# Optimization experiments

Measured on AMD Instinct MI355X. Metric: run time of the kernel, lower is better.

The kernel has to match this reference:

```python
import jax, jax.numpy as jnp
import numpy as np

EMBED_DIM = 1024
NUM_HEADS = 16
HEAD_DIM = EMBED_DIM // NUM_HEADS
SCALE = HEAD_DIM ** 0.5


def setup_inputs() -> dict:
    key = jax.random.key(0)
    kx, kq, kk, kv, ko = jax.random.split(key, 5)
    B, S, D = 4, 2048, EMBED_DIM
    std = 1.0 / np.sqrt(D)
    return {
        "x": jax.random.normal(kx, (B, S, D), dtype=jnp.float32),
        "W_q": jax.random.normal(kq, (D, D), dtype=jnp.float32) * std,
        "W_k": jax.random.normal(kk, (D, D), dtype=jnp.float32) * std,
        "W_v": jax.random.normal(kv, (D, D), dtype=jnp.float32) * std,
        "W_o": jax.random.normal(ko, (D, D), dtype=jnp.float32) * std,
    }


def reference(x, W_q, W_k, W_v, W_o):
    B, S, D = x.shape
    H, Hd = NUM_HEADS, HEAD_DIM

    def split(t):  # [B,S,D] -> [B,H,S,Hd]
        return t.reshape(B, S, H, Hd).transpose(0, 2, 1, 3)

    # nn.Linear stores weight as [out,in] and computes x @ W.T
    Q = split(x @ W_q.T)
    K = split(x @ W_k.T)
    V = split(x @ W_v.T)

    scores = jnp.einsum("bhqd,bhkd->bhqk", Q, K) / SCALE
    causal = jnp.tril(jnp.ones((S, S), dtype=bool))
    scores = jnp.where(causal, scores, -jnp.inf)
    weights = jax.nn.softmax(scores, axis=-1)  # dropout p=0 (eval)
    out = jnp.einsum("bhqk,bhkd->bhqd", weights, V)
    out = out.transpose(0, 2, 1, 3).reshape(B, S, D)
    return out @ W_o.T
```

## Files before the change

kernel.cpp:

```cpp
#include <hip/hip_runtime.h>
#include <stdint.h>

#define DEV __device__ __forceinline__

typedef __bf16 bf16x8 __attribute__((ext_vector_type(8)));
typedef float f32x4 __attribute__((ext_vector_type(4)));

DEV ushort f2bf(float f) {
    union { float f; uint32_t u; } v; v.f = f;
    uint32_t r = v.u + 0x7FFFu + ((v.u >> 16) & 1u);
    return (ushort)(r >> 16);
}

DEV ushort bfc(float f) {
    union { __bf16 h; ushort u; } v;
    v.h = (__bf16)f;
    return v.u;
}

DEV void gld16(const void* g, void* lds) {
    __builtin_amdgcn_global_load_lds(
        (const __attribute__((address_space(1))) void*)g,
        (__attribute__((address_space(3))) void*)lds, 16, 0, 0);
}

DEV bf16x8 ld_frag(const void* p) { return *(const bf16x8*)p; }

__global__ void cvt_kernel(const float* __restrict__ in, ushort* __restrict__ out, int n4) {
    int i = blockIdx.x * blockDim.x + threadIdx.x;
    if (i >= n4) return;
    float4 v = ((const float4*)in)[i];
    ushort4 o;
    o.x = f2bf(v.x); o.y = f2bf(v.y); o.z = f2bf(v.z); o.w = f2bf(v.w);
    ((ushort4*)out)[i] = o;
}

__global__ void cvt4_kernel(const float* __restrict__ w0, const float* __restrict__ w1,
                            const float* __restrict__ w2, const float* __restrict__ w3,
                            ushort* __restrict__ out, int n4) {
    int i = blockIdx.x * blockDim.x + threadIdx.x;
    if (i >= n4) return;
    const float* src = (blockIdx.y == 0) ? w0 : (blockIdx.y == 1) ? w1
                     : (blockIdx.y == 2) ? w2 : w3;
    float4 v = ((const float4*)src)[i];
    ushort4 o;
    o.x = f2bf(v.x); o.y = f2bf(v.y); o.z = f2bf(v.z); o.w = f2bf(v.w);
    ((ushort4*)(out + (size_t)blockIdx.y * n4 * 4))[i] = o;
}

template<int F32OUT>
__global__ __launch_bounds__(256) void gemm_bt(const ushort* __restrict__ A,
                                               const ushort* __restrict__ B,
                                               void* __restrict__ C,
                                               int M, int N, int K) {
    __shared__ __align__(16) ushort As[128 * 64];
    __shared__ __align__(16) ushort Bs[128 * 64];
    const int G = gridDim.x;
    const int bid = blockIdx.x;
    const int swz = (bid & 7) * (G >> 3) + (bid >> 3);
    const int bm = swz & 63, bn = swz >> 6;
    const int t = threadIdx.x, l = t & 63, w = t >> 6;
    const int wm = w >> 1, wn = w & 1;
    const int rA = l & 15, cc = l >> 4;
    f32x4 acc[4][4] = {};

    for (int k0 = 0; k0 < K; k0 += 64) {
#pragma unroll
        for (int i = 0; i < 4; ++i) {
            int o = (w * 4 + i) * 1024 + l * 16;
            int row = o >> 7, ch = (o >> 4) & 7;
            int cs = ch ^ (row & 7);
            const char* ga = (const char*)A + (((size_t)(bm * 128 + row)) * K + k0) * 2 + cs * 16;
            gld16(ga, (char*)As + (w * 4 + i) * 1024);
            const char* gb = (const char*)B + (((size_t)(bn * 128 + row)) * K + k0) * 2 + cs * 16;
            gld16(gb, (char*)Bs + (w * 4 + i) * 1024);
        }
        __syncthreads();
        bf16x8 af[4][2], bfr[4][2];
#pragma unroll
        for (int i = 0; i < 4; ++i) {
#pragma unroll
            for (int kc = 0; kc < 2; ++kc) {
                int ra = wm * 64 + i * 16 + rA;
                int ca = (kc * 4 + cc) ^ (ra & 7);
                af[i][kc] = ld_frag((const char*)As + ra * 128 + ca * 16);
                int rb = wn * 64 + i * 16 + rA;
                int cb = (kc * 4 + cc) ^ (rb & 7);
                bfr[i][kc] = ld_frag((const char*)Bs + rb * 128 + cb * 16);
            }
        }
#pragma unroll
        for (int kc = 0; kc < 2; ++kc)
#pragma unroll
            for (int i = 0; i < 4; ++i)
#pragma unroll
                for (int j = 0; j < 4; ++j)
                    acc[i][j] = __builtin_amdgcn_mfma_f32_16x16x32_bf16(
                        af[i][kc], bfr[j][kc], acc[i][j], 0, 0, 0);
        __syncthreads();
    }
#pragma unroll
    for (int i = 0; i < 4; ++i)
#pragma unroll
        for (int j = 0; j < 4; ++j)
#pragma unroll
            for (int r = 0; r < 4; ++r) {
                int row = bm * 128 + wm * 64 + i * 16 + cc * 4 + r;
                int col = bn * 128 + wn * 64 + j * 16 + rA;
                if (F32OUT) ((float*)C)[(size_t)row * N + col] = acc[i][j][r];
                else        ((ushort*)C)[(size_t)row * N + col] = f2bf(acc[i][j][r]);
            }
}

__global__ __launch_bounds__(256) void vtrans_kernel(const ushort* __restrict__ qkv,
                                                     ushort* __restrict__ vt) {
    __shared__ ushort tile[64][68];
    const int st = blockIdx.x, bh = blockIdx.y;
    const int b = bh >> 4, h = bh & 15;
    const int t = threadIdx.x;
    const ushort* src = qkv + (size_t)(b * 2048 + st * 64) * 3072 + 2048 + h * 64;
#pragma unroll
    for (int i = 0; i < 2; ++i) {
        int idx = t + i * 256;
        int s = idx >> 3, d0 = (idx & 7) * 8;
        uint4 v = *(const uint4*)(src + (size_t)s * 3072 + d0);
        *(uint2*)&tile[s][d0]     = make_uint2(v.x, v.y);
        *(uint2*)&tile[s][d0 + 4] = make_uint2(v.z, v.w);
    }
    __syncthreads();
    ushort* dst = vt + (size_t)bh * 64 * 2048 + st * 64;
#pragma unroll
    for (int i = 0; i < 2; ++i) {
        int idx = t + i * 256;
        int d = idx >> 3, s0 = (idx & 7) * 8;
        ushort tmp[8];
#pragma unroll
        for (int j = 0; j < 8; ++j) tmp[j] = tile[s0 + j][d];
        *(uint4*)(dst + (size_t)d * 2048 + s0) = *(uint4*)tmp;
    }
}

DEV void stage_kv(const char* Kg0, const char* Vg0, int kv0,
                  char* KsB, char* VsB, int t) {
    int row = t >> 3;
    int cs = (t & 7) ^ (row & 7);
    gld16(Kg0 + (size_t)(kv0 + row) * 6144 + cs * 16, KsB + t * 16);
    gld16(Vg0 + (size_t)row * 4096 + (size_t)kv0 * 2 + cs * 16, VsB + t * 16);
}

DEV void attn_tile(const char* KsB, const char* VsB, char* PsW,
                   const bf16x8* qf, f32x4* oacc, float& lsum,
                   int rA, int cc, int qg, int kv0, bool diag) {
    f32x4 s[4] = {};
    __builtin_amdgcn_s_setprio(1);
#pragma unroll
    for (int kc = 0; kc < 2; ++kc)
#pragma unroll
        for (int c = 0; c < 4; ++c) {
            int rk = c * 16 + rA;
            int ck = (kc * 4 + cc) ^ (rk & 7);
            bf16x8 ak = ld_frag(KsB + rk * 128 + ck * 16);
            s[c] = __builtin_amdgcn_mfma_f32_16x16x32_bf16(ak, qf[kc], s[c], 0, 0, 0);
        }
    __builtin_amdgcn_s_setprio(0);
    const float SC = 0.18033688011116013f;
    const int swz = (rA & 7) << 4;
#pragma unroll
    for (int c = 0; c < 4; ++c) {
        float pv[4];
#pragma unroll
        for (int r = 0; r < 4; ++r) {
            float v = s[c][r] * SC;
            if (diag && (kv0 + c * 16 + cc * 4 + r > qg)) v = -1e30f;
            pv[r] = __builtin_amdgcn_exp2f(v);
            lsum += pv[r];
        }
        union { ushort us[4]; uint2 u2; } pk;
        pk.us[0] = bfc(pv[0]); pk.us[1] = bfc(pv[1]);
        pk.us[2] = bfc(pv[2]); pk.us[3] = bfc(pv[3]);
        *(uint2*)(PsW + rA * 128 + ((32 * c + 8 * cc) ^ swz)) = pk.u2;
    }
    bf16x8 ap[2];
    ap[0] = ld_frag(PsW + rA * 128 + ((16 * cc) ^ swz));
    ap[1] = ld_frag(PsW + rA * 128 + ((64 + 16 * cc) ^ swz));
    __builtin_amdgcn_s_setprio(1);
#pragma unroll
    for (int kc = 0; kc < 2; ++kc)
#pragma unroll
        for (int g = 0; g < 4; ++g) {
            int rv = g * 16 + rA;
            int cv = (kc * 4 + cc) ^ (rv & 7);
            bf16x8 av = ld_frag(VsB + rv * 128 + cv * 16);
            oacc[g] = __builtin_amdgcn_mfma_f32_16x16x32_bf16(av, ap[kc], oacc[g], 0, 0, 0);
        }
    __builtin_amdgcn_s_setprio(0);
}

__global__ __launch_bounds__(512, 4) void attn_kernel(const ushort* __restrict__ qkv,
                                                      const ushort* __restrict__ vt,
                                                      ushort* __restrict__ o_out) {
    const int i = blockIdx.x;
    const int xcd = i & 7, slot = i >> 3;
    const int p = slot >> 3;
    const int bh = ((slot & 7) << 3) | xcd;
    const int ftq = 15 - p;
    const int b = bh >> 4, h = bh & 15;
    const int t = threadIdx.x, l = t & 63, w = t >> 6;
    const int rA = l & 15, cc = l >> 4;
    const int wq16 = w * 16;

    __shared__ __align__(16) ushort Ks[2][64 * 64];
    __shared__ __align__(16) ushort Vs[2][64 * 64];
    __shared__ __align__(16) ushort Ps[8][16 * 64];

    const size_t xbase = (size_t)(b * 2048) * 3072 + (size_t)h * 64;
    const char* Kg0 = (const char*)(qkv + xbase + 1024);
    const char* Vg0 = (const char*)(vt + (size_t)bh * 64 * 2048);

    const int qgN = p * 128 + wq16 + rA;
    const int qgF = ftq * 128 + wq16 + rA;

    bf16x8 qfN[2], qfF[2];
    {
        const ushort* qpN = qkv + xbase + (size_t)qgN * 3072;
        const ushort* qpF = qkv + xbase + (size_t)qgF * 3072;
        qfN[0] = *(const bf16x8*)(qpN + cc * 8);
        qfN[1] = *(const bf16x8*)(qpN + 32 + cc * 8);
        qfF[0] = *(const bf16x8*)(qpF + cc * 8);
        qfF[1] = *(const bf16x8*)(qpF + 32 + cc * 8);
    }
    f32x4 oN[4] = {}, oF[4] = {};
    float lN = 0.f, lF = 0.f;

    const int nkv = 32 - 2 * p;
    stage_kv(Kg0, Vg0, 0, (char*)Ks[0], (char*)Vs[0], t);
    asm volatile("s_waitcnt vmcnt(0)" ::: "memory");
    __builtin_amdgcn_s_barrier();

    for (int kt = 0; kt < nkv; ++kt) {
        const int cur = kt & 1;
        if (kt + 1 < nkv)
            stage_kv(Kg0, Vg0, (kt + 1) * 64, (char*)Ks[cur ^ 1], (char*)Vs[cur ^ 1], t);
        const char* KsB = (const char*)Ks[cur];
        const char* VsB = (const char*)Vs[cur];
        attn_tile(KsB, VsB, (char*)Ps[w], qfF, oF, lF, rA, cc, qgF, kt * 64, kt >= nkv - 2);
        if (kt <= 2 * p + 1)
            attn_tile(KsB, VsB, (char*)Ps[w], qfN, oN, lN, rA, cc, qgN, kt * 64, kt >= 2 * p);
        asm volatile("s_waitcnt vmcnt(0)" ::: "memory");
        __builtin_amdgcn_s_barrier();
    }

    float lf = lF; lf += __shfl_xor(lf, 16); lf += __shfl_xor(lf, 32);
    float ln = lN; ln += __shfl_xor(ln, 16); ln += __shfl_xor(ln, 32);
    const float rf = 1.0f / lf, rn = 1.0f / ln;
    const size_t obF = (size_t)(b * 2048 + qgF) * 1024 + h * 64;
    const size_t obN = (size_t)(b * 2048 + qgN) * 1024 + h * 64;
#pragma unroll
    for (int g = 0; g < 4; ++g) {
        union { ushort us[4]; uint2 u2; } pf, pn;
#pragma unroll
        for (int r = 0; r < 4; ++r) {
            pf.us[r] = bfc(oF[g][r] * rf);
            pn.us[r] = bfc(oN[g][r] * rn);
        }
        *(uint2*)(o_out + obF + 16 * g + 4 * cc) = pf.u2;
        *(uint2*)(o_out + obN + 16 * g + 4 * cc) = pn.u2;
    }
}

extern "C" void kernel_launch(void* const* d_in, const int* in_sizes, int n_in,
                              void* d_out, int out_size, void* d_ws, size_t ws_size,
                              hipStream_t stream) {
    const float* x  = (const float*)d_in[0];
    const float* Wq = (const float*)d_in[1];
    const float* Wk = (const float*)d_in[2];
    const float* Wv = (const float*)d_in[3];
    const float* Wo = (const float*)d_in[4];
    float* out = (float*)d_out;

    const int M = 8192, D = 1024;
    char* ws = (char*)d_ws;
    ushort* xo_bf = (ushort*)ws;
    ushort* wqkv  = (ushort*)(ws + (size_t)M * D * 2);
    ushort* wo_bf = (ushort*)(ws + (size_t)M * D * 2 + (size_t)3 * D * D * 2);
    ushort* qkv   = (ushort*)(ws + (size_t)M * D * 2 + (size_t)4 * D * D * 2);
    ushort* vt    = (ushort*)d_out;

    cvt_kernel<<<dim3(M * D / 4 / 256), 256, 0, stream>>>(x, xo_bf, M * D / 4);
    cvt4_kernel<<<dim3(D * D / 4 / 256, 4), 256, 0, stream>>>(Wq, Wk, Wv, Wo, wqkv, D * D / 4);

    gemm_bt<0><<<dim3((M / 128) * (3072 / 128)), 256, 0, stream>>>(xo_bf, wqkv, qkv, M, 3072, D);

    vtrans_kernel<<<dim3(32, 64), 256, 0, stream>>>(qkv, vt);

    attn_kernel<<<dim3(512), 512, 0, stream>>>(qkv, vt, xo_bf);

    gemm_bt<1><<<dim3((M / 128) * (D / 128)), 256, 0, stream>>>(xo_bf, wo_bf, out, M, D, D);
}
```

Measured before the change: 258.3 us.

## Use 256x256-tile double-buffered GEMM for QKV projection

Adds a new gemm256 kernel with 512 threads, 256x256 output tiles, and double-buffered LDS. Each K-tile's global loads are interleaved in four quarters between the MFMA phases, with swizzled LDS addresses. It replaces the 128x128 gemm_bt for the QKV projection to raise arithmetic intensity and overlap loads with compute. In exchange it uses more registers and LDS (128KB) per block and launches fewer blocks (384), which could hurt occupancy or tail balance.

```diff
diff --git a/kernel.cpp b/kernel.cpp
--- a/kernel.cpp
+++ b/kernel.cpp
@@ -46,6 +46,102 @@
     ushort4 o;
     o.x = f2bf(v.x); o.y = f2bf(v.y); o.z = f2bf(v.z); o.w = f2bf(v.w);
     ((ushort4*)(out + (size_t)blockIdx.y * n4 * 4))[i] = o;
+}
+
+DEV void stage_half(const ushort* Mp, int grow0, int k0, char* ldsbase, int t, int K) {
+#pragma unroll
+    for (int i = 0; i < 2; ++i) {
+        int o = (i * 512 + t) * 16;
+        int row = o >> 7;
+        int cs = ((o >> 4) & 7) ^ (row & 7);
+        gld16((const char*)Mp + ((size_t)(grow0 + row) * K + k0) * 2 + cs * 16, ldsbase + o);
+    }
+}
+
+DEV void gphase(const char* Ab, const char* Bb, f32x4 acc[8][4],
+                int wr, int wc, int rA, int cc, int mh, int nh) {
+    bf16x8 af[4][2], bg[2][2];
+#pragma unroll
+    for (int i2 = 0; i2 < 4; ++i2)
+#pragma unroll
+        for (int kc = 0; kc < 2; ++kc) {
+            int ra = wr * 128 + mh * 64 + i2 * 16 + rA;
+            af[i2][kc] = ld_frag(Ab + ra * 128 + (((kc * 4 + cc) ^ (ra & 7)) * 16));
+        }
+#pragma unroll
+    for (int j2 = 0; j2 < 2; ++j2)
+#pragma unroll
+        for (int kc = 0; kc < 2; ++kc) {
+            int rb = wc * 64 + nh * 32 + j2 * 16 + rA;
+            bg[j2][kc] = ld_frag(Bb + rb * 128 + (((kc * 4 + cc) ^ (rb & 7)) * 16));
+        }
+    __builtin_amdgcn_s_setprio(1);
+#pragma unroll
+    for (int kc = 0; kc < 2; ++kc)
+#pragma unroll
+        for (int i2 = 0; i2 < 4; ++i2)
+#pragma unroll
+            for (int j2 = 0; j2 < 2; ++j2)
+                acc[mh * 4 + i2][nh * 2 + j2] = __builtin_amdgcn_mfma_f32_16x16x32_bf16(
+                    af[i2][kc], bg[j2][kc], acc[mh * 4 + i2][nh * 2 + j2], 0, 0, 0);
+    __builtin_amdgcn_s_setprio(0);
+}
+
+template<int F32OUT>
+__global__ __launch_bounds__(512, 2) void gemm256(const ushort* __restrict__ A,
+                                                  const ushort* __restrict__ B,
+                                                  void* __restrict__ C,
+                                                  int M, int N, int K) {
+    __shared__ __align__(16) ushort S[2][2][16384];
+    const int G = gridDim.x;
+    const int bid = blockIdx.x;
+    const int swz = (bid & 7) * (G >> 3) + (bid >> 3);
+    const int nbn = N >> 8;
+    const int bm = swz / nbn, bn = swz % nbn;
+    const int t = threadIdx.x, l = t & 63, w = t >> 6;
+    const int wr = w >> 2, wc = w & 3;
+    const int rA = l & 15, cc = l >> 4;
+    f32x4 acc[8][4] = {};
+    const int NT = K >> 6;
+
+    stage_half(A, bm * 256,       0, (char*)S[0][0],         t, K);
+    stage_half(A, bm * 256 + 128, 0, (char*)S[0][0] + 16384, t, K);
+    stage_half(B, bn * 256,       0, (char*)S[0][1],         t, K);
+    stage_half(B, bn * 256 + 128, 0, (char*)S[0][1] + 16384, t, K);
+    asm volatile("s_waitcnt vmcnt(0)" ::: "memory");
+    __builtin_amdgcn_s_barrier();
+
+    for (int kt = 0; kt < NT; ++kt) {
+        const int buf = kt & 1;
+        const char* Ab = (const char*)S[buf][0];
+        const char* Bb = (const char*)S[buf][1];
+        char* An = (char*)S[buf ^ 1][0];
+        char* Bn = (char*)S[buf ^ 1][1];
+        const int k1 = (kt + 1) << 6;
+        const bool more = (kt + 1 < NT);
+        if (more) stage_half(A, bm * 256,       k1, An,         t, K);
+        gphase(Ab, Bb, acc, wr, wc, rA, cc, 0, 0);
+        if (more) stage_half(A, bm * 256 + 128, k1, An + 16384, t, K);
+        gphase(Ab, Bb, acc, wr, wc, rA, cc, 0, 1);
+        if (more) stage_half(B, bn * 256,       k1, Bn,         t, K);
+        gphase(Ab, Bb, acc, wr, wc, rA, cc, 1, 0);
+        if (more) stage_half(B, bn * 256 + 128, k1, Bn + 16384, t, K);
+        gphase(Ab, Bb, acc, wr, wc, rA, cc, 1, 1);
+        asm volatile("s_waitcnt vmcnt(0)" ::: "memory");
+        __builtin_amdgcn_s_barrier();
+    }
+
+#pragma unroll
+    for (int i = 0; i < 8; ++i)
+#pragma unroll
+        for (int j = 0; j < 4; ++j)
+#pragma unroll
+            for (int r = 0; r < 4; ++r) {
+                int row = bm * 256 + wr * 128 + i * 16 + cc * 4 + r;
+                int col = bn * 256 + wc * 64 + j * 16 + rA;
+                if (F32OUT) ((float*)C)[(size_t)row * N + col] = acc[i][j][r];
+                else        ((ushort*)C)[(size_t)row * N + col] = f2bf(acc[i][j][r]);
+            }
 }
 
 template<int F32OUT>
@@ -289,7 +385,7 @@
     cvt_kernel<<<dim3(M * D / 4 / 256), 256, 0, stream>>>(x, xo_bf, M * D / 4);
     cvt4_kernel<<<dim3(D * D / 4 / 256, 4), 256, 0, stream>>>(Wq, Wk, Wv, Wo, wqkv, D * D / 4);
 
-    gemm_bt<0><<<dim3((M / 128) * (3072 / 128)), 256, 0, stream>>>(xo_bf, wqkv, qkv, M, 3072, D);
+    gemm256<0><<<dim3((M / 256) * (3072 / 256)), 512, 0, stream>>>(xo_bf, wqkv, qkv, M, 3072, D);
 
     vtrans_kernel<<<dim3(32, 64), 256, 0, stream>>>(qkv, vt);
 
```

Measured after the change: 244.7 us. 1.06x faster.
